# Optimization experiments

Measured on AMD Instinct MI355X. Metric: run time of the kernel, lower is better.

## Reference

```python
import jax, jax.numpy as jnp
import numpy as np


def _gcn_conv(x, src, dst, W, b, n):
    """PyG GCNConv with default settings: add self-loops, symmetric norm, bias after agg.
    out = D^{-1/2} (A + I) D^{-1/2} (x @ W) + b
    """
    h = x @ W  # [N, out]
    # degree of A+I with unit edge weights: 1 (self-loop) + in-degree on dst
    deg = jnp.ones((n,), x.dtype).at[dst].add(jnp.ones((dst.shape[0],), x.dtype))
    dinv = jax.lax.rsqrt(deg)  # [N]
    coef = dinv[src] * dinv[dst]  # [E]
    agg = jax.ops.segment_sum(h[src] * coef[:, None], dst, num_segments=n)
    # self-loop contribution: norm = dinv[i]*dinv[i]
    return agg + h * (dinv * dinv)[:, None] + b


def setup_inputs() -> dict:
    key = jax.random.key(0)
    ks = jax.random.split(key, 10)
    N, E, D, H1, H2 = 100000, 2500000, 128, 32, 64
    x = jax.random.normal(ks[0], (N, D), jnp.float32)
    ei = jax.random.randint(ks[1], (2, E), 0, N, dtype=jnp.int32)
    # GCN layer params (glorot-ish scale)
    W1c = jax.random.normal(ks[2], (D, H1), jnp.float32) / np.sqrt(D)
    b1c = jnp.zeros((H1,), jnp.float32)
    W2c = jax.random.normal(ks[3], (H1, H2), jnp.float32) / np.sqrt(H1)
    b2c = jnp.zeros((H2,), jnp.float32)
    # MLP head: Linear(H2,H2) -> ReLU -> Linear(H2,1)
    Wm1 = jax.random.normal(ks[4], (H2, H2), jnp.float32) / np.sqrt(H2)
    bm1 = jnp.zeros((H2,), jnp.float32)
    Wm2 = jax.random.normal(ks[5], (H2, 1), jnp.float32) / np.sqrt(H2)
    bm2 = jnp.zeros((1,), jnp.float32)
    return {"x": x, "W1c": W1c, "b1c": b1c, "W2c": W2c, "b2c": b2c,
            "Wm1": Wm1, "bm1": bm1, "Wm2": Wm2, "bm2": bm2,
            "ei": ei, "num_nodes": 50000}


def reference(x, W1c, b1c, W2c, b2c, Wm1, bm1, Wm2, bm2, ei, num_nodes):
    src, dst = ei[0], ei[1]
    n = x.shape[0]
    z = jax.nn.relu(_gcn_conv(x, src, dst, W1c, b1c, n))
    z = jax.nn.relu(_gcn_conv(z, src, dst, W2c, b2c, n))
    v = jax.nn.relu(z @ Wm1 + bm1) @ Wm2 + bm2  # [N, 1]
    nbatches = n // num_nodes
    # mean per-graph state value (reshape over stacked graphs, mean over nodes)
    return v.reshape(nbatches, num_nodes).mean(axis=1)
```

## Files before the change

kernel.cpp:

```cpp
#include <hip/hip_runtime.h>


typedef _Float16 half_t;
typedef __attribute__((ext_vector_type(8))) _Float16 half8;
typedef __attribute__((ext_vector_type(4))) float f32x4;

#define CHUNK 8192
#define BKN   128
#define NBMAX 1024

__global__ void k_zero_out(float* out, int n) {
    int i = blockIdx.x * blockDim.x + threadIdx.x;
    if (i < n) out[i] = 0.0f;
}


__global__ __launch_bounds__(256) void k_count_coarse(
    const int* __restrict__ dst, int* __restrict__ table, int E, int nblk, int NB)
{
    __shared__ int cnt[NBMAX];
    const int tid = threadIdx.x;
    for (int i = tid; i < NB; i += 256) cnt[i] = 0;
    __syncthreads();
    const int base = blockIdx.x * CHUNK;
    const int lim = min(CHUNK, E - base);
    if (lim == CHUNK) {
        const int4* d4 = (const int4*)(dst + base);
        for (int i = tid; i < CHUNK / 4; i += 256) {
            int4 v = d4[i];
            atomicAdd(&cnt[v.x >> 7], 1);
            atomicAdd(&cnt[v.y >> 7], 1);
            atomicAdd(&cnt[v.z >> 7], 1);
            atomicAdd(&cnt[v.w >> 7], 1);
        }
    } else {
        for (int i = tid; i < lim; i += 256) atomicAdd(&cnt[dst[base + i] >> 7], 1);
    }
    __syncthreads();
    for (int b = tid; b < NB; b += 256) table[b * nblk + blockIdx.x] = cnt[b];
}

__global__ __launch_bounds__(256) void k_scan1(const int* __restrict__ cnts, int* __restrict__ S,
                                               int* __restrict__ bsums, int T) {
    __shared__ int sh[256];
    int t = threadIdx.x;
    int i = blockIdx.x * 256 + t;
    int v = (i < T) ? cnts[i] : 0;
    sh[t] = v;
    __syncthreads();
    for (int off = 1; off < 256; off <<= 1) {
        int tv = (t >= off) ? sh[t - off] : 0;
        __syncthreads();
        sh[t] += tv;
        __syncthreads();
    }
    if (i < T) S[i + 1] = sh[t];
    if (t == 255) bsums[blockIdx.x] = sh[255];
}

__global__ __launch_bounds__(1024) void k_scan2(int* bs, int nb) {
    __shared__ int sh[1024];
    int t = threadIdx.x;
    int v = (t < nb) ? bs[t] : 0;
    sh[t] = v;
    __syncthreads();
    for (int off = 1; off < 1024; off <<= 1) {
        int tv = (t >= off) ? sh[t - off] : 0;
        __syncthreads();
        sh[t] += tv;
        __syncthreads();
    }
    if (t < nb) bs[t] = sh[t] - v;
}

__global__ void k_scan3(int* __restrict__ S, const int* __restrict__ bs, int T) {
    int i = blockIdx.x * blockDim.x + threadIdx.x;
    if (i < T) S[i + 1] += bs[i >> 8];
    if (i == 0) S[0] = 0;
}

__global__ __launch_bounds__(256) void k_scatter2(
    const int* __restrict__ ei, const int* __restrict__ S,
    int* __restrict__ codes, int E, int nblk, int NB)
{
    __shared__ int cur[NBMAX];
    const int tid = threadIdx.x;
    for (int i = tid; i < NB; i += 256) cur[i] = S[i * nblk + blockIdx.x];
    __syncthreads();
    const int base = blockIdx.x * CHUNK;
    const int lim = min(CHUNK, E - base);
    if (lim == CHUNK) {
        const int4* s4 = (const int4*)(ei + base);
        const int4* d4 = (const int4*)(ei + E + base);
        for (int i = tid; i < CHUNK / 4; i += 256) {
            int4 sv = s4[i], dv = d4[i];
            {
                int pos = atomicAdd(&cur[dv.x >> 7], 1);
                codes[pos] = ((dv.x & 127) << 17) | sv.x;
            }
            {
                int pos = atomicAdd(&cur[dv.y >> 7], 1);
                codes[pos] = ((dv.y & 127) << 17) | sv.y;
            }
            {
                int pos = atomicAdd(&cur[dv.z >> 7], 1);
                codes[pos] = ((dv.z & 127) << 17) | sv.z;
            }
            {
                int pos = atomicAdd(&cur[dv.w >> 7], 1);
                codes[pos] = ((dv.w & 127) << 17) | sv.w;
            }
        }
    } else {
        for (int i = tid; i < lim; i += 256) {
            int e = base + i;
            int s = ei[e], d = ei[E + e];
            int pos = atomicAdd(&cur[d >> 7], 1);
            codes[pos] = ((d & 127) << 17) | s;
        }
    }
}

__global__ __launch_bounds__(256) void k_fine(
    const int* __restrict__ codes, const int* __restrict__ S,
    int* __restrict__ esrc, int* __restrict__ row_start,
    float* __restrict__ dinv, int nblk, int N, int E, int NB)
{
    __shared__ int cnt[BKN];
    __shared__ int sh[BKN];
    __shared__ int cur[BKN];
    const int tid = threadIdx.x;
    if (tid < BKN) cnt[tid] = 0;
    __syncthreads();
    const int b = blockIdx.x;
    const int beg = S[b * nblk], end = S[(b + 1) * nblk];
    for (int e = beg + tid; e < end; e += 256) atomicAdd(&cnt[codes[e] >> 17], 1);
    __syncthreads();
    if (tid < BKN) sh[tid] = cnt[tid];
    __syncthreads();
    for (int off = 1; off < BKN; off <<= 1) {
        int tv = (tid >= off && tid < BKN) ? sh[tid - off] : 0;
        __syncthreads();
        if (tid < BKN) sh[tid] += tv;
        __syncthreads();
    }
    if (tid < BKN) {
        int fs = beg + sh[tid] - cnt[tid];
        cur[tid] = fs;
        int n = b * BKN + tid;
        if (n < N) {
            row_start[n] = fs;
            dinv[n] = rsqrtf(1.0f + (float)cnt[tid]);
        }
    }
    if (b == NB - 1 && tid == 0) row_start[N] = E;
    __syncthreads();
    for (int e = beg + tid; e < end; e += 256) {
        int c = codes[e];
        int pos = atomicAdd(&cur[c >> 17], 1);
        esrc[pos] = c & 0x1FFFF;
    }
}


__global__ __launch_bounds__(256) void k_prep(
    const float* __restrict__ W1, const float* __restrict__ W2, const float* __restrict__ Wm1,
    half_t* __restrict__ W1t, half_t* __restrict__ W2t, half_t* __restrict__ Wm1t)
{
    int i = blockIdx.x * 256 + threadIdx.x;
    if (i < 128 * 32) { int k = i >> 5, c = i & 31; W1t[c * 128 + k] = (half_t)W1[i]; }
    if (i < 32 * 64)  { int k = i >> 6, c = i & 63; W2t[c * 32 + k]  = (half_t)W2[i]; }
    if (i < 64 * 64)  { int k = i >> 6, c = i & 63; Wm1t[c * 64 + k] = (half_t)Wm1[i]; }
}

__global__ __launch_bounds__(256) void k_gemm1_mfma(
    const float* __restrict__ x, const half_t* __restrict__ W1t,
    const float* __restrict__ dinv, half_t* __restrict__ hs1, int N)
{
    const int tid = threadIdx.x;
    const int wid = tid >> 6, lane = tid & 63;
    const int quad = lane >> 4, n16 = lane & 15;
    const int n0 = blockIdx.x * 64 + wid * 16;
    if (n0 >= N) return;
    const int nrow = min(n0 + n16, N - 1);
    const float* xr = x + (size_t)nrow * 128;
    f32x4 acc0 = {0.f, 0.f, 0.f, 0.f}, acc1 = {0.f, 0.f, 0.f, 0.f};
#pragma unroll
    for (int kc = 0; kc < 4; ++kc) {
        float4 f0 = *(const float4*)(xr + kc * 32 + quad * 8);
        float4 f1 = *(const float4*)(xr + kc * 32 + quad * 8 + 4);
        half8 a;
        a[0] = (half_t)f0.x; a[1] = (half_t)f0.y; a[2] = (half_t)f0.z; a[3] = (half_t)f0.w;
        a[4] = (half_t)f1.x; a[5] = (half_t)f1.y; a[6] = (half_t)f1.z; a[7] = (half_t)f1.w;
        half8 b0 = *(const half8*)(W1t + (size_t)n16 * 128 + kc * 32 + quad * 8);
        half8 b1 = *(const half8*)(W1t + (size_t)(16 + n16) * 128 + kc * 32 + quad * 8);
        acc0 = __builtin_amdgcn_mfma_f32_16x16x32_f16(a, b0, acc0, 0, 0, 0);
        acc1 = __builtin_amdgcn_mfma_f32_16x16x32_f16(a, b1, acc1, 0, 0, 0);
    }
#pragma unroll
    for (int r = 0; r < 4; ++r) {
        int n = n0 + quad * 4 + r;
        if (n < N) {
            float dv = dinv[n];
            hs1[(size_t)n * 32 + n16]      = (half_t)(acc0[r] * dv);
            hs1[(size_t)n * 32 + 16 + n16] = (half_t)(acc1[r] * dv);
        }
    }
}

template <bool L1>
__global__ __launch_bounds__(256) void k_aggh(
    const int* __restrict__ row_start, const int* __restrict__ esrc,
    const half_t* __restrict__ IN, const float* __restrict__ bias,
    const float* __restrict__ dinv, half_t* __restrict__ OUT, int N)
{
    const int tid = threadIdx.x;
    const int g = tid >> 2, l = tid & 3;
    const int n = blockIdx.x * 64 + g;
    if (n >= N) return;
    const half8* IN8 = (const half8*)IN;
    const int beg = row_start[n], end = row_start[n + 1];
    half8 self = IN8[(size_t)n * 4 + l];
    float acc[8];
#pragma unroll
    for (int j = 0; j < 8; ++j) acc[j] = (float)self[j];
    int e = beg;
    for (; e + 3 < end; e += 4) {
        int s0 = esrc[e], s1 = esrc[e + 1], s2 = esrc[e + 2], s3 = esrc[e + 3];
        half8 v0 = IN8[(size_t)s0 * 4 + l];
        half8 v1 = IN8[(size_t)s1 * 4 + l];
        half8 v2 = IN8[(size_t)s2 * 4 + l];
        half8 v3 = IN8[(size_t)s3 * 4 + l];
#pragma unroll
        for (int j = 0; j < 8; ++j)
            acc[j] += ((float)v0[j] + (float)v1[j]) + ((float)v2[j] + (float)v3[j]);
    }
    for (; e < end; ++e) {
        half8 v = IN8[(size_t)esrc[e] * 4 + l];
#pragma unroll
        for (int j = 0; j < 8; ++j) acc[j] += (float)v[j];
    }
    const float dv = dinv[n];
    half8 o;
    if (L1) {
#pragma unroll
        for (int j = 0; j < 8; ++j) {
            float bb = bias[l * 8 + j];
            o[j] = (half_t)(fmaxf(dv * acc[j] + bb, 0.f) * dv);
        }
    } else {
#pragma unroll
        for (int j = 0; j < 8; ++j) o[j] = (half_t)(dv * acc[j]);
    }
    ((half8*)OUT)[(size_t)n * 4 + l] = o;
}

__global__ __launch_bounds__(256) void k_tail_mfma(
    const half_t* __restrict__ Y, const half_t* __restrict__ W2t, const float* __restrict__ b2,
    const half_t* __restrict__ Wm1t, const float* __restrict__ bm1,
    const float* __restrict__ Wm2, const float* __restrict__ bm2,
    const int* __restrict__ nn_p, float* __restrict__ out, int N, int n_graphs)
{
    __shared__ float gacc[32];
    __shared__ __align__(16) half_t Hb[4][16][72];
    const int tid = threadIdx.x;
    if (tid < 32) gacc[tid] = 0.f;
    __syncthreads();
    const int wid = tid >> 6, lane = tid & 63;
    const int quad = lane >> 4, n16 = lane & 15;
    const int n0 = blockIdx.x * 64 + wid * 16;
    if (n0 < N) {
        const int nrow = min(n0 + n16, N - 1);
        half8 a1 = *(const half8*)(Y + (size_t)nrow * 32 + quad * 8);
        f32x4 acc1[4];
#pragma unroll
        for (int t = 0; t < 4; ++t) {
            half8 bf = *(const half8*)(W2t + (size_t)(t * 16 + n16) * 32 + quad * 8);
            f32x4 z = {0.f, 0.f, 0.f, 0.f};
            acc1[t] = __builtin_amdgcn_mfma_f32_16x16x32_f16(a1, bf, z, 0, 0, 0);
        }
#pragma unroll
        for (int t = 0; t < 4; ++t) {
            int c = t * 16 + n16;
            float bb = b2[c];
#pragma unroll
            for (int r = 0; r < 4; ++r)
                Hb[wid][quad * 4 + r][c] = (half_t)fmaxf(acc1[t][r] + bb, 0.f);
        }
        half8 a2lo = *(const half8*)&Hb[wid][n16][quad * 8];
        half8 a2hi = *(const half8*)&Hb[wid][n16][32 + quad * 8];
        f32x4 acc2[4];
#pragma unroll
        for (int t = 0; t < 4; ++t) {
            half8 b0 = *(const half8*)(Wm1t + (size_t)(t * 16 + n16) * 64 + quad * 8);
            half8 b1 = *(const half8*)(Wm1t + (size_t)(t * 16 + n16) * 64 + 32 + quad * 8);
            f32x4 a = {0.f, 0.f, 0.f, 0.f};
            a = __builtin_amdgcn_mfma_f32_16x16x32_f16(a2lo, b0, a, 0, 0, 0);
            a = __builtin_amdgcn_mfma_f32_16x16x32_f16(a2hi, b1, a, 0, 0, 0);
            acc2[t] = a;
        }
        float vsum[4] = {0.f, 0.f, 0.f, 0.f};
#pragma unroll
        for (int t = 0; t < 4; ++t) {
            int c = t * 16 + n16;
            float bb = bm1[c], ww = Wm2[c];
#pragma unroll
            for (int r = 0; r < 4; ++r)
                vsum[r] += fmaxf(acc2[t][r] + bb, 0.f) * ww;
        }
#pragma unroll
        for (int m = 1; m < 16; m <<= 1) {
#pragma unroll
            for (int r = 0; r < 4; ++r) vsum[r] += __shfl_xor(vsum[r], m, 64);
        }
        if (n16 == 0) {
            const int nnv = nn_p[0];
            const float bm2v = bm2[0];
#pragma unroll
            for (int r = 0; r < 4; ++r) {
                int n = n0 + quad * 4 + r;
                if (n < N) {
                    int g = n / nnv;
                    if (g < 32) atomicAdd(&gacc[g], vsum[r] + bm2v);
                }
            }
        }
    }
    __syncthreads();
    if (tid < n_graphs && tid < 32) atomicAdd(&out[tid], gacc[tid] / (float)nn_p[0]);
}

__global__ void k_zero_int(int* p, int n) {
    int i = blockIdx.x * blockDim.x + threadIdx.x;
    if (i < n) p[i] = 0;
}
__global__ void k_hist(const int* __restrict__ dst, int* __restrict__ deg, int E) {
    int e = blockIdx.x * blockDim.x + threadIdx.x;
    if (e < E) atomicAdd(&deg[dst[e]], 1);
}
__global__ void k_dinv(const int* __restrict__ deg, float* __restrict__ dinv, int n) {
    int i = blockIdx.x * blockDim.x + threadIdx.x;
    if (i < n) dinv[i] = rsqrtf(1.0f + (float)deg[i]);
}
__global__ __launch_bounds__(256) void k_gemm1f(
    const float* __restrict__ x, const float* __restrict__ W,
    const float* __restrict__ dinv, float* __restrict__ hs1, int N)
{
    __shared__ float Wl[128 * 32];
    __shared__ __align__(16) float Xl[8 * 132];
    const int tid = threadIdx.x;
    for (int i = tid; i < 128 * 32; i += 256) Wl[i] = W[i];
    const int node0 = blockIdx.x * 8;
    {
        int r = tid >> 5, c4 = tid & 31;
        int node = node0 + r;
        float4 v = make_float4(0.f, 0.f, 0.f, 0.f);
        if (node < N) v = ((const float4*)(x + (size_t)node * 128))[c4];
        *(float4*)&Xl[r * 132 + c4 * 4] = v;
    }
    __syncthreads();
    const int row = tid >> 5, f = tid & 31;
    float acc = 0.f;
#pragma unroll
    for (int k = 0; k < 128; k += 4) {
        float4 xv = *(const float4*)&Xl[row * 132 + k];
        acc += xv.x * Wl[(k + 0) * 32 + f];
        acc += xv.y * Wl[(k + 1) * 32 + f];
        acc += xv.z * Wl[(k + 2) * 32 + f];
        acc += xv.w * Wl[(k + 3) * 32 + f];
    }
    const int node = node0 + row;
    if (node < N) hs1[(size_t)node * 32 + f] = acc * dinv[node];
}
__global__ __launch_bounds__(256) void k_gemm2(
    const float* __restrict__ agg1, const float* __restrict__ W,
    const float* __restrict__ dinv, float* __restrict__ hs2, int N)
{
    __shared__ float Wl[32 * 64];
    __shared__ __align__(16) float Zl[4 * 36];
    const int tid = threadIdx.x;
    for (int i = tid; i < 32 * 64; i += 256) Wl[i] = W[i];
    const int node0 = blockIdx.x * 4;
    if (tid < 128) {
        int r = tid >> 5, c = tid & 31;
        int node = node0 + r;
        float v = 0.f;
        if (node < N) v = fmaxf(agg1[(size_t)node * 32 + c], 0.f);
        Zl[r * 36 + c] = v;
    }
    __syncthreads();
    const int row = tid >> 6, f = tid & 63;
    float acc = 0.f;
#pragma unroll
    for (int k = 0; k < 32; k += 4) {
        float4 zv = *(const float4*)&Zl[row * 36 + k];
        acc += zv.x * Wl[(k + 0) * 64 + f];
        acc += zv.y * Wl[(k + 1) * 64 + f];
        acc += zv.z * Wl[(k + 2) * 64 + f];
        acc += zv.w * Wl[(k + 3) * 64 + f];
    }
    int node = node0 + row;
    if (node < N) hs2[(size_t)node * 64 + f] = acc * dinv[node];
}
template <int F>
__global__ void k_agg_init(const float* __restrict__ hs, const float* __restrict__ b,
                           const float* __restrict__ dinv, float* __restrict__ agg, int N)
{
    long long t = (long long)blockIdx.x * blockDim.x + threadIdx.x;
    int n = (int)(t / F), f = (int)(t % F);
    if (n < N) agg[(size_t)n * F + f] = hs[(size_t)n * F + f] * dinv[n] + b[f];
}
template <int F>
__global__ void k_edge_atomic(const int* __restrict__ ei, const float* __restrict__ hs,
                              const float* __restrict__ dinv, float* __restrict__ agg, int E)
{
    long long tid = (long long)blockIdx.x * blockDim.x + threadIdx.x;
    int e = (int)(tid / F), f = (int)(tid % F);
    if (e < E) {
        int s = ei[e], d = ei[E + e];
        atomicAdd(&agg[(size_t)d * F + f], hs[(size_t)s * F + f] * dinv[d]);
    }
}
__global__ __launch_bounds__(256) void k_mlp(
    const float* __restrict__ agg2, const float* __restrict__ Wm1,
    const float* __restrict__ bm1, const float* __restrict__ Wm2,
    const float* __restrict__ bm2, float* __restrict__ vout, int N)
{
    __shared__ float Wl[64 * 64];
    __shared__ float W2l[64];
    __shared__ __align__(16) float Zl[4][64];
    const int tid = threadIdx.x;
    for (int i = tid; i < 64 * 64; i += 256) Wl[i] = Wm1[i];
    if (tid < 64) W2l[tid] = Wm2[tid];
    const int wid = tid >> 6, lane = tid & 63;
    const int node = blockIdx.x * 4 + wid;
    float zv = 0.f;
    if (node < N) zv = fmaxf(agg2[(size_t)node * 64 + lane], 0.f);
    Zl[wid][lane] = zv;
    __syncthreads();
    float t = bm1[lane];
#pragma unroll
    for (int k = 0; k < 64; k += 4) {
        float4 z4 = *(const float4*)&Zl[wid][k];
        t += z4.x * Wl[(k + 0) * 64 + lane];
        t += z4.y * Wl[(k + 1) * 64 + lane];
        t += z4.z * Wl[(k + 2) * 64 + lane];
        t += z4.w * Wl[(k + 3) * 64 + lane];
    }
    t = fmaxf(t, 0.f);
    float val = t * W2l[lane];
#pragma unroll
    for (int off = 32; off > 0; off >>= 1) val += __shfl_down(val, off, 64);
    if (lane == 0 && node < N) vout[node] = val + bm2[0];
}
__global__ void k_reduce(const float* __restrict__ v, const int* __restrict__ num_nodes_p,
                         float* out, int N, int n_graphs)
{
    __shared__ float acc[32];
    int tid = threadIdx.x;
    if (tid < n_graphs) acc[tid] = 0.f;
    __syncthreads();
    int i = blockIdx.x * blockDim.x + tid;
    int nn = num_nodes_p[0];
    if (i < N) {
        int g = i / nn;
        if (g < n_graphs) atomicAdd(&acc[g], v[i]);
    }
    __syncthreads();
    if (tid < n_graphs) atomicAdd(&out[tid], acc[tid] / (float)nn);
}

extern "C" void kernel_launch(void* const* d_in, const int* in_sizes, int n_in,
                              void* d_out, int out_size, void* d_ws, size_t ws_size,
                              hipStream_t stream)
{
    const float* x   = (const float*)d_in[0];
    const float* W1  = (const float*)d_in[1];
    const float* b1  = (const float*)d_in[2];
    const float* W2  = (const float*)d_in[3];
    const float* b2  = (const float*)d_in[4];
    const float* Wm1 = (const float*)d_in[5];
    const float* bm1 = (const float*)d_in[6];
    const float* Wm2 = (const float*)d_in[7];
    const float* bm2 = (const float*)d_in[8];
    const int*   ei  = (const int*)d_in[9];
    const int*   nn  = (const int*)d_in[10];
    const int N = in_sizes[0] / 128;
    const int E = in_sizes[9] / 2;
    float* out = (float*)d_out;

    const int NB = (N + BKN - 1) / BKN;
    const int nblk = (E + CHUNK - 1) / CHUNK;
    const long long T = (long long)NB * nblk;
    const int nb1 = (int)((T + 255) / 256);
    const size_t need_ints = (size_t)T + (size_t)(T + 1) + 1024
                           + (size_t)E + (size_t)E + (size_t)(N + 1)
                           + (size_t)N + 48ull * N + 5120;
    const bool use_new = (N <= 131072) && (T <= 262144) && (nb1 <= 1024)
                       && (out_size <= 32)
                       && (ws_size >= need_ints * sizeof(int));

    k_zero_out<<<1, 64, 0, stream>>>(out, out_size);

    if (use_new) {
        int*    table     = (int*)d_ws;
        int*    S         = table + T;
        int*    bsums     = S + (T + 1);
        int*    codes     = bsums + 1024;
        int*    esrc      = codes + E;
        int*    row_start = esrc + E;
        float*  dinv      = (float*)(row_start + N + 1);
        half_t* hs1h      = (half_t*)(dinv + N);
        half_t* Zs        = hs1h + 32 * (size_t)N;
        half_t* Y         = Zs + 32 * (size_t)N;
        half_t* W1t       = Y + 32 * (size_t)N;
        half_t* W2t       = W1t + 4096;
        half_t* Wm1t      = W2t + 2048;

        k_count_coarse<<<nblk, 256, 0, stream>>>(ei + E, table, E, nblk, NB);
        k_scan1<<<nb1, 256, 0, stream>>>(table, S, bsums, (int)T);
        k_scan2<<<1, 1024, 0, stream>>>(bsums, nb1);
        k_scan3<<<nb1, 256, 0, stream>>>(S, bsums, (int)T);
        k_scatter2<<<nblk, 256, 0, stream>>>(ei, S, codes, E, nblk, NB);
        k_fine<<<NB, 256, 0, stream>>>(codes, S, esrc, row_start, dinv, nblk, N, E, NB);
        k_prep<<<16, 256, 0, stream>>>(W1, W2, Wm1, W1t, W2t, Wm1t);
        k_gemm1_mfma<<<(N + 63) / 64, 256, 0, stream>>>(x, W1t, dinv, hs1h, N);
        k_aggh<true><<<(N + 63) / 64, 256, 0, stream>>>(row_start, esrc, hs1h, b1, dinv, Zs, N);
        k_aggh<false><<<(N + 63) / 64, 256, 0, stream>>>(row_start, esrc, Zs, b1, dinv, Y, N);
        k_tail_mfma<<<(N + 63) / 64, 256, 0, stream>>>(Y, W2t, b2, Wm1t, bm1, Wm2, bm2,
                                                       nn, out, N, out_size);
    } else {
        const size_t Ns = (size_t)N;
        float* dinv = (float*)d_ws;
        float* B    = dinv + N;
        float* hs1  = B;
        float* agg1 = B + 32 * Ns;
        float* hs2  = B + 64 * Ns;
        float* agg2 = B + 128 * Ns;
        float* vtmp = B;
        int*   deg  = (int*)B;

        const int nb = (N + 255) / 256;
        k_zero_int<<<nb, 256, 0, stream>>>(deg, N);
        k_hist<<<(E + 255) / 256, 256, 0, stream>>>(ei + E, deg, E);
        k_dinv<<<nb, 256, 0, stream>>>(deg, dinv, N);
        k_gemm1f<<<(N + 7) / 8, 256, 0, stream>>>(x, W1, dinv, hs1, N);
        {
            long long t = (long long)N * 32;
            k_agg_init<32><<<(unsigned)((t + 255) / 256), 256, 0, stream>>>(hs1, b1, dinv, agg1, N);
            t = (long long)E * 32;
            k_edge_atomic<32><<<(unsigned)((t + 255) / 256), 256, 0, stream>>>(ei, hs1, dinv, agg1, E);
        }
        k_gemm2<<<(N + 3) / 4, 256, 0, stream>>>(agg1, W2, dinv, hs2, N);
        {
            long long t = (long long)N * 64;
            k_agg_init<64><<<(unsigned)((t + 255) / 256), 256, 0, stream>>>(hs2, b2, dinv, agg2, N);
            t = (long long)E * 64;
            k_edge_atomic<64><<<(unsigned)((t + 255) / 256), 256, 0, stream>>>(ei, hs2, dinv, agg2, E);
        }
        k_mlp<<<(N + 3) / 4, 256, 0, stream>>>(agg2, Wm1, bm1, Wm2, bm2, vtmp, N);
        k_reduce<<<nb, 256, 0, stream>>>(vtmp, nn, out, N, out_size);
    }
}
```

Measured before the change: 295.8 us.

## Split gather aggregation into two source-half passes for cache locality

The fine sort now also keys each edge on whether its source node lies in the lower or upper half of the node range, and records a per-row midpoint. Aggregation runs as two passes: the first gathers only low-half sources into an fp32 accumulator buffer, the second gathers high-half sources and finishes the layer. The intent is to shrink the working set of gathered feature rows so each pass fits better in cache. This adds an extra fp32 accumulator round trip, two more kernel launches, and nontemporal hints on the streamed index and output traffic. The output zeroing is also folded into the prep kernel to save a launch.

```diff
diff --git a/kernel.cpp b/kernel.cpp
--- a/kernel.cpp
+++ b/kernel.cpp
@@ -94,22 +94,10 @@
         const int4* d4 = (const int4*)(ei + E + base);
         for (int i = tid; i < CHUNK / 4; i += 256) {
             int4 sv = s4[i], dv = d4[i];
-            {
-                int pos = atomicAdd(&cur[dv.x >> 7], 1);
-                codes[pos] = ((dv.x & 127) << 17) | sv.x;
-            }
-            {
-                int pos = atomicAdd(&cur[dv.y >> 7], 1);
-                codes[pos] = ((dv.y & 127) << 17) | sv.y;
-            }
-            {
-                int pos = atomicAdd(&cur[dv.z >> 7], 1);
-                codes[pos] = ((dv.z & 127) << 17) | sv.z;
-            }
-            {
-                int pos = atomicAdd(&cur[dv.w >> 7], 1);
-                codes[pos] = ((dv.w & 127) << 17) | sv.w;
-            }
+            { int pos = atomicAdd(&cur[dv.x >> 7], 1); codes[pos] = ((dv.x & 127) << 17) | sv.x; }
+            { int pos = atomicAdd(&cur[dv.y >> 7], 1); codes[pos] = ((dv.y & 127) << 17) | sv.y; }
+            { int pos = atomicAdd(&cur[dv.z >> 7], 1); codes[pos] = ((dv.z & 127) << 17) | sv.z; }
+            { int pos = atomicAdd(&cur[dv.w >> 7], 1); codes[pos] = ((dv.w & 127) << 17) | sv.w; }
         }
     } else {
         for (int i = tid; i < lim; i += 256) {
@@ -122,42 +110,51 @@
 }
 
 __global__ __launch_bounds__(256) void k_fine(
-    const int* __restrict__ codes, const int* __restrict__ S,
-    int* __restrict__ esrc, int* __restrict__ row_start,
+    const int* __restrict__ codes, const int* __restrict__ S, int Nhalf,
+    int* __restrict__ esrc, int* __restrict__ row_start, int* __restrict__ row_mid,
     float* __restrict__ dinv, int nblk, int N, int E, int NB)
 {
-    __shared__ int cnt[BKN];
-    __shared__ int sh[BKN];
-    __shared__ int cur[BKN];
-    const int tid = threadIdx.x;
-    if (tid < BKN) cnt[tid] = 0;
+    __shared__ int cnt[256];
+    __shared__ int sh[256];
+    __shared__ int cur[256];
+    const int tid = threadIdx.x;
+    cnt[tid] = 0;
     __syncthreads();
     const int b = blockIdx.x;
     const int beg = S[b * nblk], end = S[(b + 1) * nblk];
-    for (int e = beg + tid; e < end; e += 256) atomicAdd(&cnt[codes[e] >> 17], 1);
-    __syncthreads();
-    if (tid < BKN) sh[tid] = cnt[tid];
-    __syncthreads();
-    for (int off = 1; off < BKN; off <<= 1) {
-        int tv = (tid >= off && tid < BKN) ? sh[tid - off] : 0;
+    for (int e = beg + tid; e < end; e += 256) {
+        int c = codes[e];
+        int key = ((c >> 17) << 1) | ((c & 0x1FFFF) >= Nhalf ? 1 : 0);
+        atomicAdd(&cnt[key], 1);
+    }
+    __syncthreads();
+    sh[tid] = cnt[tid];
+    __syncthreads();
+    for (int off = 1; off < 256; off <<= 1) {
+        int tv = (tid >= off) ? sh[tid - off] : 0;
         __syncthreads();
-        if (tid < BKN) sh[tid] += tv;
+        sh[tid] += tv;
         __syncthreads();
     }
-    if (tid < BKN) {
+    {
         int fs = beg + sh[tid] - cnt[tid];
         cur[tid] = fs;
-        int n = b * BKN + tid;
+        int n = b * BKN + (tid >> 1);
         if (n < N) {
-            row_start[n] = fs;
-            dinv[n] = rsqrtf(1.0f + (float)cnt[tid]);
+            if ((tid & 1) == 0) {
+                row_start[n] = fs;
+                dinv[n] = rsqrtf(1.0f + (float)(cnt[tid] + cnt[tid + 1]));
+            } else {
+                row_mid[n] = fs;
+            }
         }
     }
     if (b == NB - 1 && tid == 0) row_start[N] = E;
     __syncthreads();
     for (int e = beg + tid; e < end; e += 256) {
         int c = codes[e];
-        int pos = atomicAdd(&cur[c >> 17], 1);
+        int key = ((c >> 17) << 1) | ((c & 0x1FFFF) >= Nhalf ? 1 : 0);
+        int pos = atomicAdd(&cur[key], 1);
         esrc[pos] = c & 0x1FFFF;
     }
 }
@@ -165,12 +162,14 @@
 
 __global__ __launch_bounds__(256) void k_prep(
     const float* __restrict__ W1, const float* __restrict__ W2, const float* __restrict__ Wm1,
-    half_t* __restrict__ W1t, half_t* __restrict__ W2t, half_t* __restrict__ Wm1t)
+    half_t* __restrict__ W1t, half_t* __restrict__ W2t, half_t* __restrict__ Wm1t,
+    float* __restrict__ out, int out_n)
 {
     int i = blockIdx.x * 256 + threadIdx.x;
     if (i < 128 * 32) { int k = i >> 5, c = i & 31; W1t[c * 128 + k] = (half_t)W1[i]; }
     if (i < 32 * 64)  { int k = i >> 6, c = i & 63; W2t[c * 32 + k]  = (half_t)W2[i]; }
     if (i < 64 * 64)  { int k = i >> 6, c = i & 63; Wm1t[c * 64 + k] = (half_t)Wm1[i]; }
+    if (i < out_n) out[i] = 0.0f;
 }
 
 __global__ __launch_bounds__(256) void k_gemm1_mfma(
@@ -208,25 +207,27 @@
     }
 }
 
-template <bool L1>
-__global__ __launch_bounds__(256) void k_aggh(
-    const int* __restrict__ row_start, const int* __restrict__ esrc,
-    const half_t* __restrict__ IN, const float* __restrict__ bias,
-    const float* __restrict__ dinv, half_t* __restrict__ OUT, int N)
+__global__ __launch_bounds__(256) void k_agg_p0(
+    const int* __restrict__ row_start, const int* __restrict__ row_mid,
+    const int* __restrict__ esrc, const half_t* __restrict__ IN,
+    float* __restrict__ accf, int N)
 {
     const int tid = threadIdx.x;
     const int g = tid >> 2, l = tid & 3;
     const int n = blockIdx.x * 64 + g;
     if (n >= N) return;
     const half8* IN8 = (const half8*)IN;
-    const int beg = row_start[n], end = row_start[n + 1];
+    const int beg = row_start[n], mid = row_mid[n];
     half8 self = IN8[(size_t)n * 4 + l];
     float acc[8];
 #pragma unroll
     for (int j = 0; j < 8; ++j) acc[j] = (float)self[j];
     int e = beg;
-    for (; e + 3 < end; e += 4) {
-        int s0 = esrc[e], s1 = esrc[e + 1], s2 = esrc[e + 2], s3 = esrc[e + 3];
+    for (; e + 3 < mid; e += 4) {
+        int s0 = __builtin_nontemporal_load(esrc + e);
+        int s1 = __builtin_nontemporal_load(esrc + e + 1);
+        int s2 = __builtin_nontemporal_load(esrc + e + 2);
+        int s3 = __builtin_nontemporal_load(esrc + e + 3);
         half8 v0 = IN8[(size_t)s0 * 4 + l];
         half8 v1 = IN8[(size_t)s1 * 4 + l];
         half8 v2 = IN8[(size_t)s2 * 4 + l];
@@ -235,8 +236,49 @@
         for (int j = 0; j < 8; ++j)
             acc[j] += ((float)v0[j] + (float)v1[j]) + ((float)v2[j] + (float)v3[j]);
     }
+    for (; e < mid; ++e) {
+        half8 v = IN8[(size_t)__builtin_nontemporal_load(esrc + e) * 4 + l];
+#pragma unroll
+        for (int j = 0; j < 8; ++j) acc[j] += (float)v[j];
+    }
+    f32x4 o0 = {acc[0], acc[1], acc[2], acc[3]};
+    f32x4 o1 = {acc[4], acc[5], acc[6], acc[7]};
+    __builtin_nontemporal_store(o0, (f32x4*)(accf + (size_t)n * 32 + l * 8));
+    __builtin_nontemporal_store(o1, (f32x4*)(accf + (size_t)n * 32 + l * 8 + 4));
+}
+
+template <bool L1>
+__global__ __launch_bounds__(256) void k_agg_p1(
+    const int* __restrict__ row_start, const int* __restrict__ row_mid,
+    const int* __restrict__ esrc, const half_t* __restrict__ IN,
+    const float* __restrict__ accf, const float* __restrict__ bias,
+    const float* __restrict__ dinv, half_t* __restrict__ OUT, int N)
+{
+    const int tid = threadIdx.x;
+    const int g = tid >> 2, l = tid & 3;
+    const int n = blockIdx.x * 64 + g;
+    if (n >= N) return;
+    const half8* IN8 = (const half8*)IN;
+    const int mid = row_mid[n], end = row_start[n + 1];
+    f32x4 a0 = __builtin_nontemporal_load((const f32x4*)(accf + (size_t)n * 32 + l * 8));
+    f32x4 a1 = __builtin_nontemporal_load((const f32x4*)(accf + (size_t)n * 32 + l * 8 + 4));
+    float acc[8] = {a0[0], a0[1], a0[2], a0[3], a1[0], a1[1], a1[2], a1[3]};
+    int e = mid;
+    for (; e + 3 < end; e += 4) {
+        int s0 = __builtin_nontemporal_load(esrc + e);
+        int s1 = __builtin_nontemporal_load(esrc + e + 1);
+        int s2 = __builtin_nontemporal_load(esrc + e + 2);
+        int s3 = __builtin_nontemporal_load(esrc + e + 3);
+        half8 v0 = IN8[(size_t)s0 * 4 + l];
+        half8 v1 = IN8[(size_t)s1 * 4 + l];
+        half8 v2 = IN8[(size_t)s2 * 4 + l];
+        half8 v3 = IN8[(size_t)s3 * 4 + l];
+#pragma unroll
+        for (int j = 0; j < 8; ++j)
+            acc[j] += ((float)v0[j] + (float)v1[j]) + ((float)v2[j] + (float)v3[j]);
+    }
     for (; e < end; ++e) {
-        half8 v = IN8[(size_t)esrc[e] * 4 + l];
+        half8 v = IN8[(size_t)__builtin_nontemporal_load(esrc + e) * 4 + l];
 #pragma unroll
         for (int j = 0; j < 8; ++j) acc[j] += (float)v[j];
     }
@@ -252,7 +294,7 @@
 #pragma unroll
         for (int j = 0; j < 8; ++j) o[j] = (half_t)(dv * acc[j]);
     }
-    ((half8*)OUT)[(size_t)n * 4 + l] = o;
+    __builtin_nontemporal_store(o, (half8*)(OUT + (size_t)n * 32 + l * 8));
 }
 
 __global__ __launch_bounds__(256) void k_tail_mfma(
@@ -495,12 +537,10 @@
     const int nb1 = (int)((T + 255) / 256);
     const size_t need_ints = (size_t)T + (size_t)(T + 1) + 1024
                            + (size_t)E + (size_t)E + (size_t)(N + 1)
-                           + (size_t)N + 48ull * N + 5120;
+                           + (size_t)N + (size_t)N + 32ull * N + 48ull * N + 5120;
     const bool use_new = (N <= 131072) && (T <= 262144) && (nb1 <= 1024)
-                       && (out_size <= 32)
+                       && (out_size <= 32) && ((E & 3) == 0)
                        && (ws_size >= need_ints * sizeof(int));
-
-    k_zero_out<<<1, 64, 0, stream>>>(out, out_size);
 
     if (use_new) {
         int*    table     = (int*)d_ws;
@@ -509,26 +549,35 @@
         int*    codes     = bsums + 1024;
         int*    esrc      = codes + E;
         int*    row_start = esrc + E;
-        float*  dinv      = (float*)(row_start + N + 1);
-        half_t* hs1h      = (half_t*)(dinv + N);
+        int*    row_mid   = row_start + (N + 1);
+        float*  dinv      = (float*)(row_mid + N);
+        float*  accf      = dinv + N;
+        half_t* hs1h      = (half_t*)(accf + 32 * (size_t)N);
         half_t* Zs        = hs1h + 32 * (size_t)N;
         half_t* Y         = Zs + 32 * (size_t)N;
         half_t* W1t       = Y + 32 * (size_t)N;
         half_t* W2t       = W1t + 4096;
         half_t* Wm1t      = W2t + 2048;
+        const int Nhalf = N / 2;
+        const int agrid = (N + 63) / 64;
 
         k_count_coarse<<<nblk, 256, 0, stream>>>(ei + E, table, E, nblk, NB);
         k_scan1<<<nb1, 256, 0, stream>>>(table, S, bsums, (int)T);
         k_scan2<<<1, 1024, 0, stream>>>(bsums, nb1);
         k_scan3<<<nb1, 256, 0, stream>>>(S, bsums, (int)T);
         k_scatter2<<<nblk, 256, 0, stream>>>(ei, S, codes, E, nblk, NB);
-        k_fine<<<NB, 256, 0, stream>>>(codes, S, esrc, row_start, dinv, nblk, N, E, NB);
-        k_prep<<<16, 256, 0, stream>>>(W1, W2, Wm1, W1t, W2t, Wm1t);
-        k_gemm1_mfma<<<(N + 63) / 64, 256, 0, stream>>>(x, W1t, dinv, hs1h, N);
-        k_aggh<true><<<(N + 63) / 64, 256, 0, stream>>>(row_start, esrc, hs1h, b1, dinv, Zs, N);
-        k_aggh<false><<<(N + 63) / 64, 256, 0, stream>>>(row_start, esrc, Zs, b1, dinv, Y, N);
-        k_tail_mfma<<<(N + 63) / 64, 256, 0, stream>>>(Y, W2t, b2, Wm1t, bm1, Wm2, bm2,
-                                                       nn, out, N, out_size);
+        k_fine<<<NB, 256, 0, stream>>>(codes, S, Nhalf, esrc, row_start, row_mid,
+                                       dinv, nblk, N, E, NB);
+        k_prep<<<16, 256, 0, stream>>>(W1, W2, Wm1, W1t, W2t, Wm1t, out, out_size);
+        k_gemm1_mfma<<<agrid, 256, 0, stream>>>(x, W1t, dinv, hs1h, N);
+        k_agg_p0<<<agrid, 256, 0, stream>>>(row_start, row_mid, esrc, hs1h, accf, N);
+        k_agg_p1<true><<<agrid, 256, 0, stream>>>(row_start, row_mid, esrc, hs1h,
+                                                  accf, b1, dinv, Zs, N);
+        k_agg_p0<<<agrid, 256, 0, stream>>>(row_start, row_mid, esrc, Zs, accf, N);
+        k_agg_p1<false><<<agrid, 256, 0, stream>>>(row_start, row_mid, esrc, Zs,
+                                                   accf, b1, dinv, Y, N);
+        k_tail_mfma<<<agrid, 256, 0, stream>>>(Y, W2t, b2, Wm1t, bm1, Wm2, bm2,
+                                               nn, out, N, out_size);
     } else {
         const size_t Ns = (size_t)N;
         float* dinv = (float*)d_ws;
@@ -541,6 +590,7 @@
         int*   deg  = (int*)B;
 
         const int nb = (N + 255) / 256;
+        k_zero_out<<<1, 64, 0, stream>>>(out, out_size);
         k_zero_int<<<nb, 256, 0, stream>>>(deg, N);
         k_hist<<<(E + 255) / 256, 256, 0, stream>>>(ei + E, deg, E);
         k_dinv<<<nb, 256, 0, stream>>>(deg, dinv, N);
```

After: 308.6 us. 4.3% more time.

## Widen CSR fine buckets to 512 nodes, fuse output zeroing, use nontemporal edge loads

Applied to the files above, without the earlier changes.

The two-level counting sort now groups destinations into 512-node buckets instead of 128, so there are fewer coarse buckets (NB≈196). That shrinks the per-chunk count table, the scan work and the scatter's shared cursor array, and k_fine moves to 512 threads per block. Output zeroing moves into k_prep, removing one kernel launch on the fast path. The aggregation kernels use nontemporal loads for edge indices and nontemporal stores for outputs. The trade-off is fewer, larger k_fine blocks with a longer 512-element scan, which may reduce parallelism in that stage.

```diff
diff --git a/kernel.cpp b/kernel.cpp
--- a/kernel.cpp
+++ b/kernel.cpp
@@ -6,8 +6,8 @@
 typedef __attribute__((ext_vector_type(4))) float f32x4;
 
 #define CHUNK 8192
-#define BKN   128
-#define NBMAX 1024
+#define BKN   512
+#define NBMAX 256
 
 __global__ void k_zero_out(float* out, int n) {
     int i = blockIdx.x * blockDim.x + threadIdx.x;
@@ -28,13 +28,13 @@
         const int4* d4 = (const int4*)(dst + base);
         for (int i = tid; i < CHUNK / 4; i += 256) {
             int4 v = d4[i];
-            atomicAdd(&cnt[v.x >> 7], 1);
-            atomicAdd(&cnt[v.y >> 7], 1);
-            atomicAdd(&cnt[v.z >> 7], 1);
-            atomicAdd(&cnt[v.w >> 7], 1);
+            atomicAdd(&cnt[v.x >> 9], 1);
+            atomicAdd(&cnt[v.y >> 9], 1);
+            atomicAdd(&cnt[v.z >> 9], 1);
+            atomicAdd(&cnt[v.w >> 9], 1);
         }
     } else {
-        for (int i = tid; i < lim; i += 256) atomicAdd(&cnt[dst[base + i] >> 7], 1);
+        for (int i = tid; i < lim; i += 256) atomicAdd(&cnt[dst[base + i] >> 9], 1);
     }
     __syncthreads();
     for (int b = tid; b < NB; b += 256) table[b * nblk + blockIdx.x] = cnt[b];
@@ -94,34 +94,22 @@
         const int4* d4 = (const int4*)(ei + E + base);
         for (int i = tid; i < CHUNK / 4; i += 256) {
             int4 sv = s4[i], dv = d4[i];
-            {
-                int pos = atomicAdd(&cur[dv.x >> 7], 1);
-                codes[pos] = ((dv.x & 127) << 17) | sv.x;
-            }
-            {
-                int pos = atomicAdd(&cur[dv.y >> 7], 1);
-                codes[pos] = ((dv.y & 127) << 17) | sv.y;
-            }
-            {
-                int pos = atomicAdd(&cur[dv.z >> 7], 1);
-                codes[pos] = ((dv.z & 127) << 17) | sv.z;
-            }
-            {
-                int pos = atomicAdd(&cur[dv.w >> 7], 1);
-                codes[pos] = ((dv.w & 127) << 17) | sv.w;
-            }
+            { int pos = atomicAdd(&cur[dv.x >> 9], 1); codes[pos] = ((dv.x & 511) << 17) | sv.x; }
+            { int pos = atomicAdd(&cur[dv.y >> 9], 1); codes[pos] = ((dv.y & 511) << 17) | sv.y; }
+            { int pos = atomicAdd(&cur[dv.z >> 9], 1); codes[pos] = ((dv.z & 511) << 17) | sv.z; }
+            { int pos = atomicAdd(&cur[dv.w >> 9], 1); codes[pos] = ((dv.w & 511) << 17) | sv.w; }
         }
     } else {
         for (int i = tid; i < lim; i += 256) {
             int e = base + i;
             int s = ei[e], d = ei[E + e];
-            int pos = atomicAdd(&cur[d >> 7], 1);
-            codes[pos] = ((d & 127) << 17) | s;
-        }
-    }
-}
-
-__global__ __launch_bounds__(256) void k_fine(
+            int pos = atomicAdd(&cur[d >> 9], 1);
+            codes[pos] = ((d & 511) << 17) | s;
+        }
+    }
+}
+
+__global__ __launch_bounds__(512) void k_fine(
     const int* __restrict__ codes, const int* __restrict__ S,
     int* __restrict__ esrc, int* __restrict__ row_start,
     float* __restrict__ dinv, int nblk, int N, int E, int NB)
@@ -130,21 +118,21 @@
     __shared__ int sh[BKN];
     __shared__ int cur[BKN];
     const int tid = threadIdx.x;
-    if (tid < BKN) cnt[tid] = 0;
+    cnt[tid] = 0;
     __syncthreads();
     const int b = blockIdx.x;
     const int beg = S[b * nblk], end = S[(b + 1) * nblk];
-    for (int e = beg + tid; e < end; e += 256) atomicAdd(&cnt[codes[e] >> 17], 1);
-    __syncthreads();
-    if (tid < BKN) sh[tid] = cnt[tid];
-    __syncthreads();
-    for (int off = 1; off < BKN; off <<= 1) {
-        int tv = (tid >= off && tid < BKN) ? sh[tid - off] : 0;
+    for (int e = beg + tid; e < end; e += 512) atomicAdd(&cnt[codes[e] >> 17], 1);
+    __syncthreads();
+    sh[tid] = cnt[tid];
+    __syncthreads();
+    for (int off = 1; off < 512; off <<= 1) {
+        int tv = (tid >= off) ? sh[tid - off] : 0;
         __syncthreads();
-        if (tid < BKN) sh[tid] += tv;
+        sh[tid] += tv;
         __syncthreads();
     }
-    if (tid < BKN) {
+    {
         int fs = beg + sh[tid] - cnt[tid];
         cur[tid] = fs;
         int n = b * BKN + tid;
@@ -155,7 +143,7 @@
     }
     if (b == NB - 1 && tid == 0) row_start[N] = E;
     __syncthreads();
-    for (int e = beg + tid; e < end; e += 256) {
+    for (int e = beg + tid; e < end; e += 512) {
         int c = codes[e];
         int pos = atomicAdd(&cur[c >> 17], 1);
         esrc[pos] = c & 0x1FFFF;
@@ -165,12 +153,14 @@
 
 __global__ __launch_bounds__(256) void k_prep(
     const float* __restrict__ W1, const float* __restrict__ W2, const float* __restrict__ Wm1,
-    half_t* __restrict__ W1t, half_t* __restrict__ W2t, half_t* __restrict__ Wm1t)
+    half_t* __restrict__ W1t, half_t* __restrict__ W2t, half_t* __restrict__ Wm1t,
+    float* __restrict__ out, int out_n)
 {
     int i = blockIdx.x * 256 + threadIdx.x;
     if (i < 128 * 32) { int k = i >> 5, c = i & 31; W1t[c * 128 + k] = (half_t)W1[i]; }
     if (i < 32 * 64)  { int k = i >> 6, c = i & 63; W2t[c * 32 + k]  = (half_t)W2[i]; }
     if (i < 64 * 64)  { int k = i >> 6, c = i & 63; Wm1t[c * 64 + k] = (half_t)Wm1[i]; }
+    if (i < out_n) out[i] = 0.0f;
 }
 
 __global__ __launch_bounds__(256) void k_gemm1_mfma(
@@ -226,7 +216,10 @@
     for (int j = 0; j < 8; ++j) acc[j] = (float)self[j];
     int e = beg;
     for (; e + 3 < end; e += 4) {
-        int s0 = esrc[e], s1 = esrc[e + 1], s2 = esrc[e + 2], s3 = esrc[e + 3];
+        int s0 = __builtin_nontemporal_load(esrc + e);
+        int s1 = __builtin_nontemporal_load(esrc + e + 1);
+        int s2 = __builtin_nontemporal_load(esrc + e + 2);
+        int s3 = __builtin_nontemporal_load(esrc + e + 3);
         half8 v0 = IN8[(size_t)s0 * 4 + l];
         half8 v1 = IN8[(size_t)s1 * 4 + l];
         half8 v2 = IN8[(size_t)s2 * 4 + l];
@@ -236,7 +229,7 @@
             acc[j] += ((float)v0[j] + (float)v1[j]) + ((float)v2[j] + (float)v3[j]);
     }
     for (; e < end; ++e) {
-        half8 v = IN8[(size_t)esrc[e] * 4 + l];
+        half8 v = IN8[(size_t)__builtin_nontemporal_load(esrc + e) * 4 + l];
 #pragma unroll
         for (int j = 0; j < 8; ++j) acc[j] += (float)v[j];
     }
@@ -252,7 +245,7 @@
 #pragma unroll
         for (int j = 0; j < 8; ++j) o[j] = (half_t)(dv * acc[j]);
     }
-    ((half8*)OUT)[(size_t)n * 4 + l] = o;
+    __builtin_nontemporal_store(o, (half8*)(OUT + (size_t)n * 32 + l * 8));
 }
 
 __global__ __launch_bounds__(256) void k_tail_mfma(
@@ -497,10 +490,8 @@
                            + (size_t)E + (size_t)E + (size_t)(N + 1)
                            + (size_t)N + 48ull * N + 5120;
     const bool use_new = (N <= 131072) && (T <= 262144) && (nb1 <= 1024)
-                       && (out_size <= 32)
+                       && (NB <= NBMAX) && (out_size <= 32)
                        && (ws_size >= need_ints * sizeof(int));
-
-    k_zero_out<<<1, 64, 0, stream>>>(out, out_size);
 
     if (use_new) {
         int*    table     = (int*)d_ws;
@@ -516,19 +507,20 @@
         half_t* W1t       = Y + 32 * (size_t)N;
         half_t* W2t       = W1t + 4096;
         half_t* Wm1t      = W2t + 2048;
+        const int agrid = (N + 63) / 64;
 
         k_count_coarse<<<nblk, 256, 0, stream>>>(ei + E, table, E, nblk, NB);
         k_scan1<<<nb1, 256, 0, stream>>>(table, S, bsums, (int)T);
         k_scan2<<<1, 1024, 0, stream>>>(bsums, nb1);
         k_scan3<<<nb1, 256, 0, stream>>>(S, bsums, (int)T);
         k_scatter2<<<nblk, 256, 0, stream>>>(ei, S, codes, E, nblk, NB);
-        k_fine<<<NB, 256, 0, stream>>>(codes, S, esrc, row_start, dinv, nblk, N, E, NB);
-        k_prep<<<16, 256, 0, stream>>>(W1, W2, Wm1, W1t, W2t, Wm1t);
-        k_gemm1_mfma<<<(N + 63) / 64, 256, 0, stream>>>(x, W1t, dinv, hs1h, N);
-        k_aggh<true><<<(N + 63) / 64, 256, 0, stream>>>(row_start, esrc, hs1h, b1, dinv, Zs, N);
-        k_aggh<false><<<(N + 63) / 64, 256, 0, stream>>>(row_start, esrc, Zs, b1, dinv, Y, N);
-        k_tail_mfma<<<(N + 63) / 64, 256, 0, stream>>>(Y, W2t, b2, Wm1t, bm1, Wm2, bm2,
-                                                       nn, out, N, out_size);
+        k_fine<<<NB, 512, 0, stream>>>(codes, S, esrc, row_start, dinv, nblk, N, E, NB);
+        k_prep<<<16, 256, 0, stream>>>(W1, W2, Wm1, W1t, W2t, Wm1t, out, out_size);
+        k_gemm1_mfma<<<agrid, 256, 0, stream>>>(x, W1t, dinv, hs1h, N);
+        k_aggh<true><<<agrid, 256, 0, stream>>>(row_start, esrc, hs1h, b1, dinv, Zs, N);
+        k_aggh<false><<<agrid, 256, 0, stream>>>(row_start, esrc, Zs, b1, dinv, Y, N);
+        k_tail_mfma<<<agrid, 256, 0, stream>>>(Y, W2t, b2, Wm1t, bm1, Wm2, bm2,
+                                               nn, out, N, out_size);
     } else {
         const size_t Ns = (size_t)N;
         float* dinv = (float*)d_ws;
@@ -541,6 +533,7 @@
         int*   deg  = (int*)B;
 
         const int nb = (N + 255) / 256;
+        k_zero_out<<<1, 64, 0, stream>>>(out, out_size);
         k_zero_int<<<nb, 256, 0, stream>>>(deg, N);
         k_hist<<<(E + 255) / 256, 256, 0, stream>>>(ei + E, deg, E);
         k_dinv<<<nb, 256, 0, stream>>>(deg, dinv, N);
```

Measured after the change: 293.6 us. Within noise of the previous version (-0.7%).
